# Kernel tuning notes

Hardware: AMD Instinct MI355X
Metric: run time of the kernel (lower is better)

The kernel has to match this reference:

```python
import jax, jax.numpy as jnp
import numpy as np

D_MODEL = 1024
N_HEADS = 16
HEAD_DIM = D_MODEL // N_HEADS
SCALE = HEAD_DIM ** -0.5
NEG = -9e15


def setup_inputs() -> dict:
    key = jax.random.key(0)
    k1, k2, k3 = jax.random.split(key, 3)
    B, S = 4, 2048
    x = jax.random.normal(k1, (B, S, D_MODEL), dtype=jnp.float32)
    W_qkv = jax.random.normal(k2, (D_MODEL, 3 * D_MODEL), dtype=jnp.float32) * (D_MODEL ** -0.5)
    b_qkv = jnp.zeros((3 * D_MODEL,), dtype=jnp.float32)
    W_out = jax.random.normal(k3, (D_MODEL, D_MODEL), dtype=jnp.float32) * (D_MODEL ** -0.5)
    b_out = jnp.zeros((D_MODEL,), dtype=jnp.float32)
    return {"x": x, "W_qkv": W_qkv, "b_qkv": b_qkv, "W_out": W_out, "b_out": b_out}


def reference(x, W_qkv, b_qkv, W_out, b_out):
    B, S, _ = x.shape
    qkv = x @ W_qkv + b_qkv                      # [B,S,3D]
    q, k, v = jnp.split(qkv, 3, axis=-1)
    def heads(t):
        return t.reshape(B, S, N_HEADS, HEAD_DIM).transpose(0, 2, 1, 3)  # [B,H,S,d]
    q, k, v = heads(q), heads(k), heads(v)
    logits = jnp.einsum('bhqd,bhkd->bhqk', q, k) * SCALE
    causal = jnp.tril(jnp.ones((S, S), dtype=bool))
    logits = jnp.where(causal[None, None], logits, jnp.float32(NEG))
    attn = jax.nn.softmax(logits, axis=-1)       # dropout p=0 -> identity
    vals = jnp.einsum('bhqk,bhkd->bhqd', attn, v)
    vals = vals.transpose(0, 2, 1, 3).reshape(B, S, D_MODEL)
    return vals @ W_out + b_out
```

## Files before the change

### kernel.cpp

```cpp
#include <hip/hip_runtime.h>

typedef unsigned short u16;
typedef unsigned int u32;
typedef __attribute__((ext_vector_type(8))) short bf16x8;
typedef __attribute__((ext_vector_type(4))) float f32x4;

#define MFMA16(a, b, c) __builtin_amdgcn_mfma_f32_16x16x32_bf16((a), (b), (c), 0, 0, 0)

constexpr int D = 1024;
constexpr int NH = 16;
constexpr int HD = 64;
constexpr int BB = 4;
constexpr int SS = 2048;
constexpr int BH = BB * NH;
constexpr int MTOK = BB * SS;
constexpr float SCALE_LOG2E = 0.125f * 1.44269504088896340736f;

__device__ __forceinline__ u16 f32_bf16(float f) {
  union { float f; u32 u; } v; v.f = f;
  u32 u = v.u;
  u += 0x7FFFu + ((u >> 16) & 1u);
  return (u16)(u >> 16);
}

__device__ __forceinline__ float exp2_fast(float x) {
  float r; asm("v_exp_f32 %0, %1" : "=v"(r) : "v"(x)); return r;
}
__device__ __forceinline__ u16 cvt_bf16_1(float f) {
  u32 r; asm("v_cvt_pk_bf16_f32 %0, %1, %1" : "=v"(r) : "v"(f)); return (u16)r;
}
__device__ __forceinline__ u32 cvt_pk2(float lo, float hi) {
  u32 r; asm("v_cvt_pk_bf16_f32 %0, %1, %2" : "=v"(r) : "v"(lo), "v"(hi)); return r;
}

__device__ __forceinline__ void gload_lds16(const void* g, u16* l) {
  __builtin_amdgcn_global_load_lds(
      (const __attribute__((address_space(1))) u32*)g,
      (__attribute__((address_space(3))) u32*)l, 16, 0, 0);
}

__global__ __launch_bounds__(256)
void cvt_bf16(const float* __restrict__ in, u16* __restrict__ out, int n4) {
  int i = blockIdx.x * 256 + threadIdx.x;
  const int stride = gridDim.x * 256;
  for (; i < n4; i += stride) {
    float4 v = reinterpret_cast<const float4*>(in)[i];
    u32 lo = (u32)f32_bf16(v.x) | ((u32)f32_bf16(v.y) << 16);
    u32 hi = (u32)f32_bf16(v.z) | ((u32)f32_bf16(v.w) << 16);
    reinterpret_cast<uint2*>(out)[i] = make_uint2(lo, hi);
  }
}

__global__ __launch_bounds__(256)
void transpose_bf16(const float* __restrict__ in, u16* __restrict__ out, int R, int C) {
  __shared__ float tile[32][33];
  const int c0 = blockIdx.x * 32, r0 = blockIdx.y * 32;
  const int tx = threadIdx.x, ty = threadIdx.y;
#pragma unroll
  for (int i = 0; i < 4; i++)
    tile[ty + 8 * i][tx] = in[(size_t)(r0 + ty + 8 * i) * C + c0 + tx];
  __syncthreads();
#pragma unroll
  for (int i = 0; i < 4; i++)
    out[(size_t)(c0 + ty + 8 * i) * R + r0 + tx] = f32_bf16(tile[tx][ty + 8 * i]);
}

template <int MODE>
__global__ __launch_bounds__(256)
void gemm_bf16(const u16* __restrict__ A, const u16* __restrict__ Bt,
               const float* __restrict__ bias,
               u16* __restrict__ q_out, u16* __restrict__ k_out,
               u16* __restrict__ vt_out, float* __restrict__ f_out,
               int M, int N, int K) {
  constexpr int BK = 32;
  __shared__ u16 lds_a[3][128 * BK];
  __shared__ u16 lds_b[3][128 * BK];
  const int m0 = blockIdx.x * 128;
  const int n0 = blockIdx.y * 128;
  const int t = threadIdx.x;
  const int lane = t & 63;
  const int w = t >> 6;
  const int wr = w >> 1, wc = w & 1;
  const int fr = lane & 15, fq = lane >> 4;

  const int srow = t >> 2;
  const int schunk = (t & 3) ^ ((srow >> 1) & 3);
  const u16* ga0 = A + (size_t)(m0 + srow) * K + schunk * 8;
  const u16* ga1 = ga0 + (size_t)64 * K;
  const u16* gb0 = Bt + (size_t)(n0 + srow) * K + schunk * 8;
  const u16* gb1 = gb0 + (size_t)64 * K;

  const int swz = ((fr >> 1) & 3) << 4;

#define GSTAGE(bufi, koff)                                                    \
  {                                                                           \
    gload_lds16(ga0 + (koff), lds_a[bufi] + t * 8);                           \
    gload_lds16(ga1 + (koff), lds_a[bufi] + (t + 256) * 8);                   \
    gload_lds16(gb0 + (koff), lds_b[bufi] + t * 8);                           \
    gload_lds16(gb1 + (koff), lds_b[bufi] + (t + 256) * 8);                   \
  }

  f32x4 acc[4][4] = {};
  const int nt = K / BK;

  GSTAGE(0, 0);
  GSTAGE(1, BK);

  int cur = 0;
  for (int kt = 0; kt < nt; ++kt) {
    if (kt + 1 < nt)
      asm volatile("s_waitcnt vmcnt(4)" ::: "memory");
    else
      asm volatile("s_waitcnt vmcnt(0)" ::: "memory");
    __builtin_amdgcn_s_barrier();
    __builtin_amdgcn_sched_barrier(0);

    const char* ca = (const char*)lds_a[cur];
    const char* cb = (const char*)lds_b[cur];
    bf16x8 af[4], bfr[4];
#pragma unroll
    for (int i = 0; i < 4; i++)
      af[i] = *reinterpret_cast<const bf16x8*>(
          ca + (wr * 64 + i * 16 + fr) * 64 + ((fq * 16) ^ swz));
#pragma unroll
    for (int i = 0; i < 4; i++)
      bfr[i] = *reinterpret_cast<const bf16x8*>(
          cb + (wc * 64 + i * 16 + fr) * 64 + ((fq * 16) ^ swz));
    __builtin_amdgcn_s_setprio(1);
#pragma unroll
    for (int i = 0; i < 4; i++)
#pragma unroll
      for (int j = 0; j < 4; j++)
        acc[i][j] = MFMA16(af[i], bfr[j], acc[i][j]);
    __builtin_amdgcn_s_setprio(0);

    if (kt + 2 < nt) {
      const int bufn = cur >= 1 ? cur - 1 : 2;
      GSTAGE(bufn, (kt + 2) * BK);
    }
    cur = cur == 2 ? 0 : cur + 1;
  }
#undef GSTAGE

#pragma unroll
  for (int i = 0; i < 4; i++) {
#pragma unroll
    for (int j = 0; j < 4; j++) {
      const int ncol = n0 + wc * 64 + j * 16 + fr;
      const float bs = bias[ncol];
#pragma unroll
      for (int r = 0; r < 4; r++) {
        const int mrow = m0 + wr * 64 + i * 16 + fq * 4 + r;
        const float vv = acc[i][j][r] + bs;
        if (MODE == 0) {
          const int which = ncol >> 10;
          const int rem = ncol & 1023;
          const int hh = rem >> 6, dd = rem & 63;
          const int bb = mrow >> 11, ss = mrow & 2047;
          const int bh = bb * 16 + hh;
          if (which == 0)
            q_out[((size_t)bh * SS + ss) * HD + dd] = f32_bf16(vv * SCALE_LOG2E);
          else if (which == 1)
            k_out[((size_t)bh * SS + ss) * HD + dd] = f32_bf16(vv);
          else
            vt_out[((size_t)bh * HD + dd) * SS + ss] = f32_bf16(vv);
        } else {
          f_out[(size_t)mrow * N + ncol] = vv;
        }
      }
    }
  }
}

__global__ __launch_bounds__(512)
void attn_fwd(const u16* __restrict__ Qb, const u16* __restrict__ Kb,
              const u16* __restrict__ Vt, u16* __restrict__ vals) {
  const int bid = blockIdx.x;
  const int wk = (bid & 7) * 64 + (bid >> 3);
  const int bh = wk >> 3;
  const int pA = wk & 7;
  const int qtA = pA, qtB = 15 - pA;
  const int nA = 2 * qtA + 2;
  const int nTot = 34;
  const u16* Qp = Qb + (size_t)bh * SS * HD;
  const char* Kp = (const char*)(Kb + (size_t)bh * SS * HD);
  const char* Vp = (const char*)(Vt + (size_t)bh * HD * SS);
  const int t = threadIdx.x, lane = t & 63, w = t >> 6;
  const int fr = lane & 15, fq = lane >> 4;
  const int swz = (fr & 7) << 4;

  __shared__ u16 kbuf[3][4096];
  __shared__ u16 vbuf[3][4096];
  __shared__ u16 plds[8][16][72];
  u16* myp = &plds[w][0][0];

  const int lin = t * 16;

  int offKV[8];
#pragma unroll
  for (int kf = 0; kf < 4; kf++)
#pragma unroll
    for (int kk = 0; kk < 2; kk++)
      offKV[kf * 2 + kk] = (kf * 16 + fr) * 128 + ((kk * 64 + fq * 16) ^ swz);

  bf16x8 aq[2];
  {
    const int qbase = qtA * 128 + w * 16;
#pragma unroll
    for (int kk = 0; kk < 2; kk++)
      aq[kk] = *reinterpret_cast<const bf16x8*>(Qp + (size_t)(qbase + fr) * HD + kk * 32 + fq * 8);
  }

  f32x4 o[4] = {};
  float mrun = -3e38f, lpart = 0.f;

#define STAGE(bufi, kvt_)                                                     \
  {                                                                           \
    const int row = lin >> 7, colb = lin & 127;                               \
    const int scol = colb ^ ((row & 7) << 4);                                 \
    gload_lds16(Kp + (size_t)((kvt_) * 64 + row) * 128 + scol,                \
                &kbuf[bufi][lin >> 1]);                                       \
    gload_lds16(Vp + (size_t)row * 4096 + (kvt_) * 128 + scol,                \
                &vbuf[bufi][lin >> 1]);                                       \
  }
#define KVIDX(ti_) ((ti_) >= nA ? (ti_) - nA : (ti_))

  auto write_out = [&](int qt) {
    const int b_ = bh >> 4, h_ = bh & 15;
    const int qb = qt * 128 + w * 16;
    float rs = lpart;
    rs += __shfl_xor(rs, 16, 64);
    rs += __shfl_xor(rs, 32, 64);
    const float linv = 1.f / rs;
    float lj[4];
#pragma unroll
    for (int j = 0; j < 4; j++)
      lj[j] = __shfl(linv, (lane & 48) + fq * 4 + j, 64);
#pragma unroll
    for (int df = 0; df < 4; df++)
#pragma unroll
      for (int j = 0; j < 4; j++) {
        const float vv = o[df][j] * lj[j];
        const int qg = qb + fq * 4 + j;
        vals[((size_t)(b_ * SS + qg)) * D + h_ * HD + df * 16 + fr] = cvt_bf16_1(vv);
      }
  };

  int cur = 0;
  STAGE(0, 0);
  STAGE(1, 1);

  for (int ti = 0; ti < nTot; ++ti) {
    const bool segB = ti >= nA;
    const int kvt = segB ? ti - nA : ti;
    const int qt = segB ? qtB : qtA;

    if (ti + 1 < nTot)
      asm volatile("s_waitcnt vmcnt(2)" ::: "memory");
    else
      asm volatile("s_waitcnt vmcnt(0)" ::: "memory");
    __builtin_amdgcn_s_barrier();
    __builtin_amdgcn_sched_barrier(0);

    if (ti == nA) {
      write_out(qtA);
      const int qbase = qtB * 128 + w * 16;
#pragma unroll
      for (int kk = 0; kk < 2; kk++)
        aq[kk] = *reinterpret_cast<const bf16x8*>(Qp + (size_t)(qbase + fr) * HD + kk * 32 + fq * 8);
      mrun = -3e38f; lpart = 0.f;
#pragma unroll
      for (int df = 0; df < 4; df++) o[df] = f32x4{0.f, 0.f, 0.f, 0.f};
    }

    const char* kb = (const char*)kbuf[cur];
    const char* vb = (const char*)vbuf[cur];

    f32x4 sc[4] = {};
    __builtin_amdgcn_s_setprio(1);
#pragma unroll
    for (int kf = 0; kf < 4; kf++) {
#pragma unroll
      for (int kk = 0; kk < 2; kk++) {
        bf16x8 bk = *reinterpret_cast<const bf16x8*>(kb + offKV[kf * 2 + kk]);
        sc[kf] = MFMA16(bk, aq[kk], sc[kf]);
      }
    }
    __builtin_amdgcn_s_setprio(0);
    if ((kvt >> 1) == qt) {
      const int qg = qt * 128 + w * 16 + fr;
      const int kg0 = kvt * 64 + fq * 4;
#pragma unroll
      for (int kf = 0; kf < 4; kf++)
#pragma unroll
        for (int j = 0; j < 4; j++)
          if (kg0 + kf * 16 + j > qg) sc[kf][j] = -3e38f;
    }
    float m = fmaxf(fmaxf(sc[0][0], sc[0][1]), fmaxf(sc[0][2], sc[0][3]));
#pragma unroll
    for (int kf = 1; kf < 4; kf++)
      m = fmaxf(m, fmaxf(fmaxf(sc[kf][0], sc[kf][1]), fmaxf(sc[kf][2], sc[kf][3])));
    m = fmaxf(m, __shfl_xor(m, 16, 64));
    m = fmaxf(m, __shfl_xor(m, 32, 64));
    if (__any((int)(m > mrun + 8.f))) {
      const float mnew = fmaxf(mrun, m);
      const float alpha = exp2_fast(mrun - mnew);
      mrun = mnew;
      lpart *= alpha;
      float aj[4];
#pragma unroll
      for (int j = 0; j < 4; j++)
        aj[j] = __shfl(alpha, (lane & 48) + fq * 4 + j, 64);
#pragma unroll
      for (int df = 0; df < 4; df++)
#pragma unroll
        for (int j = 0; j < 4; j++) o[df][j] *= aj[j];
    }
#pragma unroll
    for (int kf = 0; kf < 4; kf++)
#pragma unroll
      for (int j = 0; j < 4; j++) {
        const float p = exp2_fast(sc[kf][j] - mrun);
        sc[kf][j] = p;
        lpart += p;
      }
    {
      u16* mypr = myp + fr * 72;
#pragma unroll
      for (int kf = 0; kf < 4; kf++) {
        const u32 p01 = cvt_pk2(sc[kf][0], sc[kf][1]);
        const u32 p23 = cvt_pk2(sc[kf][2], sc[kf][3]);
        *reinterpret_cast<u32*>(mypr + kf * 16 + fq * 4) = p01;
        *reinterpret_cast<u32*>(mypr + kf * 16 + fq * 4 + 2) = p23;
      }
    }
    bf16x8 pa[2];
#pragma unroll
    for (int kk = 0; kk < 2; kk++)
      pa[kk] = *reinterpret_cast<const bf16x8*>(myp + fr * 72 + kk * 32 + fq * 8);
    __builtin_amdgcn_s_setprio(1);
#pragma unroll
    for (int df = 0; df < 4; df++) {
#pragma unroll
      for (int kk = 0; kk < 2; kk++) {
        bf16x8 bv = *reinterpret_cast<const bf16x8*>(vb + offKV[df * 2 + kk]);
        o[df] = MFMA16(pa[kk], bv, o[df]);
      }
    }
    __builtin_amdgcn_s_setprio(0);

    const int nxt = ti + 2;
    if (nxt < nTot) {
      const int bufn = cur >= 1 ? cur - 1 : 2;
      STAGE(bufn, KVIDX(nxt));
    }
    cur = cur == 2 ? 0 : cur + 1;
  }
  write_out(qtB);
#undef STAGE
#undef KVIDX
}

extern "C" void kernel_launch(void* const* d_in, const int* in_sizes, int n_in,
                              void* d_out, int out_size, void* d_ws, size_t ws_size,
                              hipStream_t stream) {
  const float* x = (const float*)d_in[0];
  const float* Wqkv = (const float*)d_in[1];
  const float* bqkv = (const float*)d_in[2];
  const float* Wout = (const float*)d_in[3];
  const float* bout = (const float*)d_in[4];
  float* out = (float*)d_out;

  char* p = (char*)d_ws;
  u16* xb = (u16*)p;    p += (size_t)MTOK * D * 2;
  u16* wqkvT = (u16*)p; p += (size_t)3 * D * D * 2;
  u16* woutT = (u16*)p; p += (size_t)D * D * 2;
  u16* Qb = (u16*)p;    p += (size_t)BH * SS * HD * 2;
  u16* Kb = (u16*)p;    p += (size_t)BH * SS * HD * 2;
  u16* Vt = (u16*)p;    p += (size_t)BH * SS * HD * 2;
  u16* vals = (u16*)p;  p += (size_t)MTOK * D * 2;

  cvt_bf16<<<2048, 256, 0, stream>>>(x, xb, MTOK * D / 4);
  transpose_bf16<<<dim3(3 * D / 32, D / 32), dim3(32, 8), 0, stream>>>(Wqkv, wqkvT, D, 3 * D);
  transpose_bf16<<<dim3(D / 32, D / 32), dim3(32, 8), 0, stream>>>(Wout, woutT, D, D);
  gemm_bf16<0><<<dim3(MTOK / 128, 3 * D / 128), 256, 0, stream>>>(
      xb, wqkvT, bqkv, Qb, Kb, Vt, nullptr, MTOK, 3 * D, D);
  attn_fwd<<<dim3(512), 512, 0, stream>>>(Qb, Kb, Vt, vals);
  gemm_bf16<1><<<dim3(MTOK / 128, D / 128), 256, 0, stream>>>(
      vals, woutT, bout, nullptr, nullptr, nullptr, out, MTOK, D, D);
}
```

Before: 171.8 us.

## Load GEMM B operand directly from global into registers, bypassing LDS

Stops staging the B (weight) tile in shared memory: each wave now loads its B fragments straight from global memory into registers, one k-step ahead, using double-buffered register sets. The A tile keeps its triple-buffered LDS pipeline, and the loop is unrolled by two to alternate the register buffers. This removes the B-side LDS traffic and halves the GEMM's shared-memory footprint, which could allow higher occupancy. In exchange, waves that share a column block load the same B data redundantly, the global access pattern is less coalesced (64-byte row segments), and register pressure rises.

```diff
diff --git a/kernel.cpp b/kernel.cpp
--- a/kernel.cpp
+++ b/kernel.cpp
@@ -74,7 +74,6 @@
                int M, int N, int K) {
   constexpr int BK = 32;
   __shared__ u16 lds_a[3][128 * BK];
-  __shared__ u16 lds_b[3][128 * BK];
   const int m0 = blockIdx.x * 128;
   const int n0 = blockIdx.y * 128;
   const int t = threadIdx.x;
@@ -87,60 +86,70 @@
   const int schunk = (t & 3) ^ ((srow >> 1) & 3);
   const u16* ga0 = A + (size_t)(m0 + srow) * K + schunk * 8;
   const u16* ga1 = ga0 + (size_t)64 * K;
-  const u16* gb0 = Bt + (size_t)(n0 + srow) * K + schunk * 8;
-  const u16* gb1 = gb0 + (size_t)64 * K;
+
+  const u16* gb[4];
+#pragma unroll
+  for (int j = 0; j < 4; j++)
+    gb[j] = Bt + (size_t)(n0 + wc * 64 + j * 16 + fr) * K + fq * 8;
 
   const int swz = ((fr >> 1) & 3) << 4;
 
-#define GSTAGE(bufi, koff)                                                    \
+#define ASTAGE(bufi, koff)                                                    \
   {                                                                           \
     gload_lds16(ga0 + (koff), lds_a[bufi] + t * 8);                           \
     gload_lds16(ga1 + (koff), lds_a[bufi] + (t + 256) * 8);                   \
-    gload_lds16(gb0 + (koff), lds_b[bufi] + t * 8);                           \
-    gload_lds16(gb1 + (koff), lds_b[bufi] + (t + 256) * 8);                   \
   }
 
   f32x4 acc[4][4] = {};
   const int nt = K / BK;
 
-  GSTAGE(0, 0);
-  GSTAGE(1, BK);
+  bf16x8 b0[4], b1[4];
+#pragma unroll
+  for (int j = 0; j < 4; j++)
+    b0[j] = *reinterpret_cast<const bf16x8*>(gb[j]);
+  ASTAGE(0, 0);
+  ASTAGE(1, BK);
 
   int cur = 0;
-  for (int kt = 0; kt < nt; ++kt) {
-    if (kt + 1 < nt)
-      asm volatile("s_waitcnt vmcnt(4)" ::: "memory");
-    else
-      asm volatile("s_waitcnt vmcnt(0)" ::: "memory");
-    __builtin_amdgcn_s_barrier();
-    __builtin_amdgcn_sched_barrier(0);
-
-    const char* ca = (const char*)lds_a[cur];
-    const char* cb = (const char*)lds_b[cur];
-    bf16x8 af[4], bfr[4];
-#pragma unroll
-    for (int i = 0; i < 4; i++)
-      af[i] = *reinterpret_cast<const bf16x8*>(
-          ca + (wr * 64 + i * 16 + fr) * 64 + ((fq * 16) ^ swz));
-#pragma unroll
-    for (int i = 0; i < 4; i++)
-      bfr[i] = *reinterpret_cast<const bf16x8*>(
-          cb + (wc * 64 + i * 16 + fr) * 64 + ((fq * 16) ^ swz));
-    __builtin_amdgcn_s_setprio(1);
-#pragma unroll
-    for (int i = 0; i < 4; i++)
-#pragma unroll
-      for (int j = 0; j < 4; j++)
-        acc[i][j] = MFMA16(af[i], bfr[j], acc[i][j]);
-    __builtin_amdgcn_s_setprio(0);
-
-    if (kt + 2 < nt) {
-      const int bufn = cur >= 1 ? cur - 1 : 2;
-      GSTAGE(bufn, (kt + 2) * BK);
-    }
-    cur = cur == 2 ? 0 : cur + 1;
-  }
-#undef GSTAGE
+#define GSTEP(kt, BUSE, BNEXT)                                                \
+  {                                                                           \
+    if ((kt) + 1 < nt)                                                        \
+      asm volatile("s_waitcnt vmcnt(6)" ::: "memory");                        \
+    else                                                                      \
+      asm volatile("s_waitcnt vmcnt(4)" ::: "memory");                        \
+    __builtin_amdgcn_s_barrier();                                             \
+    __builtin_amdgcn_sched_barrier(0);                                        \
+    if ((kt) + 1 < nt) {                                                      \
+      _Pragma("unroll")                                                       \
+      for (int j = 0; j < 4; j++)                                             \
+        BNEXT[j] = *reinterpret_cast<const bf16x8*>(gb[j] + ((kt) + 1) * BK); \
+    }                                                                         \
+    if ((kt) + 2 < nt) {                                                      \
+      const int bufn = cur >= 1 ? cur - 1 : 2;                 \
+      ASTAGE(bufn, ((kt) + 2) * BK);                                          \
+    }                                                                         \
+    const char* ca = (const char*)lds_a[cur];                                 \
+    bf16x8 af[4];                                                             \
+    _Pragma("unroll")                                                         \
+    for (int i = 0; i < 4; i++)                                               \
+      af[i] = *reinterpret_cast<const bf16x8*>(                               \
+          ca + (wr * 64 + i * 16 + fr) * 64 + ((fq * 16) ^ swz));             \
+    __builtin_amdgcn_s_setprio(1);                                            \
+    _Pragma("unroll")                                                         \
+    for (int i = 0; i < 4; i++)                                               \
+      _Pragma("unroll")                                                       \
+      for (int j = 0; j < 4; j++)                                             \
+        acc[i][j] = MFMA16(af[i], BUSE[j], acc[i][j]);                        \
+    __builtin_amdgcn_s_setprio(0);                                            \
+    cur = cur == 2 ? 0 : cur + 1;                                             \
+  }
+
+  for (int kt = 0; kt < nt; kt += 2) {
+    GSTEP(kt, b0, b1);
+    GSTEP(kt + 1, b1, b0);
+  }
+#undef GSTEP
+#undef ASTAGE
 
 #pragma unroll
   for (int i = 0; i < 4; i++) {
```

After: 231.8 us. +34.9%, slower.

## Enlarge GEMM tiles to 256x128 with BK=64 double buffering and vectorized V^T stores

Applied to the files above, without the earlier changes.

Moves the GEMM kernel from a 128x128 tile with 256 threads and a 3-stage BK=32 pipeline to a 256x128 tile with 512 threads and a 2-stage BK=64 pipeline. Each barrier now covers two k-substeps, and each B tile is reused across more rows of A. The QKV epilogue selects the output type once per block and packs the four V^T values into a single 8-byte store. The trade-offs are a shallower prefetch pipeline, more LDS per block (96KB), and half as many blocks, which may reduce occupancy.

```diff
diff --git a/kernel.cpp b/kernel.cpp
--- a/kernel.cpp
+++ b/kernel.cpp
@@ -66,16 +66,16 @@
 }
 
 template <int MODE>
-__global__ __launch_bounds__(256)
+__global__ __launch_bounds__(512)
 void gemm_bf16(const u16* __restrict__ A, const u16* __restrict__ Bt,
                const float* __restrict__ bias,
                u16* __restrict__ q_out, u16* __restrict__ k_out,
                u16* __restrict__ vt_out, float* __restrict__ f_out,
                int M, int N, int K) {
-  constexpr int BK = 32;
-  __shared__ u16 lds_a[3][128 * BK];
-  __shared__ u16 lds_b[3][128 * BK];
-  const int m0 = blockIdx.x * 128;
+  constexpr int BK = 64;
+  __shared__ u16 lds_a[2][16384];
+  __shared__ u16 lds_b[2][8192];
+  const int m0 = blockIdx.x * 256;
   const int n0 = blockIdx.y * 128;
   const int t = threadIdx.x;
   const int lane = t & 63;
@@ -84,32 +84,41 @@
   const int fr = lane & 15, fq = lane >> 4;
 
   const int srow = t >> 2;
-  const int schunk = (t & 3) ^ ((srow >> 1) & 3);
+  const int schunk = (t & 3) ^ ((t >> 3) & 3);
   const u16* ga0 = A + (size_t)(m0 + srow) * K + schunk * 8;
-  const u16* ga1 = ga0 + (size_t)64 * K;
+  const u16* ga1 = A + (size_t)(m0 + 128 + srow) * K + schunk * 8;
+  const u16* ga2 = ga0 + 32;
+  const u16* ga3 = ga1 + 32;
   const u16* gb0 = Bt + (size_t)(n0 + srow) * K + schunk * 8;
-  const u16* gb1 = gb0 + (size_t)64 * K;
-
-  const int swz = ((fr >> 1) & 3) << 4;
-
-#define GSTAGE(bufi, koff)                                                    \
+  const u16* gb1 = gb0 + 32;
+  const int t8 = t * 8;
+
+  const int rswz = ((fr >> 1) & 3) << 4;
+
+#define GSTAGE(bufi, kt)                                                      \
   {                                                                           \
-    gload_lds16(ga0 + (koff), lds_a[bufi] + t * 8);                           \
-    gload_lds16(ga1 + (koff), lds_a[bufi] + (t + 256) * 8);                   \
-    gload_lds16(gb0 + (koff), lds_b[bufi] + t * 8);                           \
-    gload_lds16(gb1 + (koff), lds_b[bufi] + (t + 256) * 8);                   \
+    const int ko = (kt)*BK;                                                   \
+    gload_lds16(ga0 + ko, lds_a[bufi] + t8);                                  \
+    gload_lds16(ga1 + ko, lds_a[bufi] + 4096 + t8);                           \
+    gload_lds16(ga2 + ko, lds_a[bufi] + 8192 + t8);                           \
+    gload_lds16(ga3 + ko, lds_a[bufi] + 12288 + t8);                          \
+    gload_lds16(gb0 + ko, lds_b[bufi] + t8);                                  \
+    gload_lds16(gb1 + ko, lds_b[bufi] + 4096 + t8);                           \
   }
 
   f32x4 acc[4][4] = {};
   const int nt = K / BK;
 
   GSTAGE(0, 0);
-  GSTAGE(1, BK);
-
   int cur = 0;
   for (int kt = 0; kt < nt; ++kt) {
+    if (kt) {
+      __builtin_amdgcn_s_barrier();
+      __builtin_amdgcn_sched_barrier(0);
+    }
+    if (kt + 1 < nt) GSTAGE(cur ^ 1, kt + 1);
     if (kt + 1 < nt)
-      asm volatile("s_waitcnt vmcnt(4)" ::: "memory");
+      asm volatile("s_waitcnt vmcnt(6)" ::: "memory");
     else
       asm volatile("s_waitcnt vmcnt(0)" ::: "memory");
     __builtin_amdgcn_s_barrier();
@@ -117,55 +126,70 @@
 
     const char* ca = (const char*)lds_a[cur];
     const char* cb = (const char*)lds_b[cur];
-    bf16x8 af[4], bfr[4];
-#pragma unroll
-    for (int i = 0; i < 4; i++)
-      af[i] = *reinterpret_cast<const bf16x8*>(
-          ca + (wr * 64 + i * 16 + fr) * 64 + ((fq * 16) ^ swz));
-#pragma unroll
-    for (int i = 0; i < 4; i++)
-      bfr[i] = *reinterpret_cast<const bf16x8*>(
-          cb + (wc * 64 + i * 16 + fr) * 64 + ((fq * 16) ^ swz));
-    __builtin_amdgcn_s_setprio(1);
-#pragma unroll
-    for (int i = 0; i < 4; i++)
+#pragma unroll
+    for (int ks = 0; ks < 2; ks++) {
+      bf16x8 af[4], bf[4];
+#pragma unroll
+      for (int i = 0; i < 4; i++)
+        af[i] = *reinterpret_cast<const bf16x8*>(
+            ca + ks * 16384 + (wr * 64 + i * 16 + fr) * 64 + ((fq * 16) ^ rswz));
 #pragma unroll
       for (int j = 0; j < 4; j++)
-        acc[i][j] = MFMA16(af[i], bfr[j], acc[i][j]);
-    __builtin_amdgcn_s_setprio(0);
-
-    if (kt + 2 < nt) {
-      const int bufn = cur >= 1 ? cur - 1 : 2;
-      GSTAGE(bufn, (kt + 2) * BK);
-    }
-    cur = cur == 2 ? 0 : cur + 1;
+        bf[j] = *reinterpret_cast<const bf16x8*>(
+            cb + ks * 8192 + (wc * 64 + j * 16 + fr) * 64 + ((fq * 16) ^ rswz));
+      __builtin_amdgcn_s_setprio(1);
+#pragma unroll
+      for (int i = 0; i < 4; i++)
+#pragma unroll
+        for (int j = 0; j < 4; j++)
+          acc[i][j] = MFMA16(af[i], bf[j], acc[i][j]);
+      __builtin_amdgcn_s_setprio(0);
+    }
+    cur ^= 1;
   }
 #undef GSTAGE
 
-#pragma unroll
-  for (int i = 0; i < 4; i++) {
-#pragma unroll
-    for (int j = 0; j < 4; j++) {
-      const int ncol = n0 + wc * 64 + j * 16 + fr;
-      const float bs = bias[ncol];
-#pragma unroll
-      for (int r = 0; r < 4; r++) {
-        const int mrow = m0 + wr * 64 + i * 16 + fq * 4 + r;
-        const float vv = acc[i][j][r] + bs;
-        if (MODE == 0) {
-          const int which = ncol >> 10;
-          const int rem = ncol & 1023;
-          const int hh = rem >> 6, dd = rem & 63;
-          const int bb = mrow >> 11, ss = mrow & 2047;
-          const int bh = bb * 16 + hh;
-          if (which == 0)
-            q_out[((size_t)bh * SS + ss) * HD + dd] = f32_bf16(vv * SCALE_LOG2E);
-          else if (which == 1)
-            k_out[((size_t)bh * SS + ss) * HD + dd] = f32_bf16(vv);
-          else
-            vt_out[((size_t)bh * HD + dd) * SS + ss] = f32_bf16(vv);
+  if (MODE == 0) {
+    const int swhich = n0 >> 10;
+#pragma unroll
+    for (int i = 0; i < 4; i++) {
+#pragma unroll
+      for (int j = 0; j < 4; j++) {
+        const int ncol = n0 + wc * 64 + j * 16 + fr;
+        const float bs = bias[ncol];
+        const int rem = ncol & 1023;
+        const int hh = rem >> 6, dd = rem & 63;
+        const int mbase = m0 + wr * 64 + i * 16 + fq * 4;
+        const int bb = mbase >> 11, ss = mbase & 2047;
+        const int bh = bb * 16 + hh;
+        if (swhich == 0) {
+#pragma unroll
+          for (int r = 0; r < 4; r++)
+            q_out[((size_t)bh * SS + ss + r) * HD + dd] =
+                f32_bf16((acc[i][j][r] + bs) * SCALE_LOG2E);
+        } else if (swhich == 1) {
+#pragma unroll
+          for (int r = 0; r < 4; r++)
+            k_out[((size_t)bh * SS + ss + r) * HD + dd] = f32_bf16(acc[i][j][r] + bs);
         } else {
-          f_out[(size_t)mrow * N + ncol] = vv;
+          const u32 p01 = cvt_pk2(acc[i][j][0] + bs, acc[i][j][1] + bs);
+          const u32 p23 = cvt_pk2(acc[i][j][2] + bs, acc[i][j][3] + bs);
+          *reinterpret_cast<uint2*>(&vt_out[((size_t)bh * HD + dd) * SS + ss]) =
+              make_uint2(p01, p23);
+        }
+      }
+    }
+  } else {
+#pragma unroll
+    for (int i = 0; i < 4; i++) {
+#pragma unroll
+      for (int j = 0; j < 4; j++) {
+        const int ncol = n0 + wc * 64 + j * 16 + fr;
+        const float bs = bias[ncol];
+#pragma unroll
+        for (int r = 0; r < 4; r++) {
+          const int mrow = m0 + wr * 64 + i * 16 + fq * 4 + r;
+          f_out[(size_t)mrow * N + ncol] = acc[i][j][r] + bs;
         }
       }
     }
@@ -383,9 +407,9 @@
   cvt_bf16<<<2048, 256, 0, stream>>>(x, xb, MTOK * D / 4);
   transpose_bf16<<<dim3(3 * D / 32, D / 32), dim3(32, 8), 0, stream>>>(Wqkv, wqkvT, D, 3 * D);
   transpose_bf16<<<dim3(D / 32, D / 32), dim3(32, 8), 0, stream>>>(Wout, woutT, D, D);
-  gemm_bf16<0><<<dim3(MTOK / 128, 3 * D / 128), 256, 0, stream>>>(
+  gemm_bf16<0><<<dim3(MTOK / 256, 3 * D / 128), 512, 0, stream>>>(
       xb, wqkvT, bqkv, Qb, Kb, Vt, nullptr, MTOK, 3 * D, D);
   attn_fwd<<<dim3(512), 512, 0, stream>>>(Qb, Kb, Vt, vals);
-  gemm_bf16<1><<<dim3(MTOK / 128, D / 128), 256, 0, stream>>>(
+  gemm_bf16<1><<<dim3(MTOK / 256, D / 128), 512, 0, stream>>>(
       vals, woutT, bout, nullptr, nullptr, nullptr, out, MTOK, D, D);
 }
```

Result: slower. 179.0 us (+4.2%).

## Replace QKV GEMM with 256x256-tile 8-wave kernel using phased async LDS prefetch

Applied to the files above, without the earlier changes.

Adds a dedicated QKV projection kernel that uses 256x256 output tiles, 512 threads and BK=64, with an XOR-swizzled LDS layout. Each k-step is split into four quarter-phases, and each phase issues the next staging load directly from global memory to LDS, so loads overlap with MFMA work across double buffers. The intent is more data reuse per block and better latency hiding than the 128x128 generic GEMM. In exchange the kernel carries 128 accumulators per thread, which raises register pressure and lowers occupancy, and the grid is only 32x12 blocks.

```diff
diff --git a/kernel.cpp b/kernel.cpp
--- a/kernel.cpp
+++ b/kernel.cpp
@@ -63,6 +63,125 @@
 #pragma unroll
   for (int i = 0; i < 4; i++)
     out[(size_t)(c0 + ty + 8 * i) * R + r0 + tx] = f32_bf16(tile[tx][ty + 8 * i]);
+}
+
+__global__ __launch_bounds__(512)
+void gemm_qkv_8ph(const u16* __restrict__ A, const u16* __restrict__ Bt,
+                  const float* __restrict__ bias,
+                  u16* __restrict__ q_out, u16* __restrict__ k_out,
+                  u16* __restrict__ vt_out) {
+  constexpr int K = 1024, BK = 64, NT = K / BK;
+  __shared__ u16 ldsA[2][2][128 * 64];
+  __shared__ u16 ldsB[2][2][128 * 64];
+  const int m0 = blockIdx.x * 256;
+  const int n0 = blockIdx.y * 256;
+  const int t = threadIdx.x, lane = t & 63, w = t >> 6;
+  const int wr = w >> 2, wc = w & 3;
+  const int fr = lane & 15, fq = lane >> 4;
+  const int rsw = fr & 7;
+
+  const int srow = t >> 3;
+  const int sch = (t & 7) ^ (srow & 7);
+  const u16* gA0 = A + (size_t)(m0 + srow) * K + sch * 8;
+  const u16* gA1 = A + (size_t)(m0 + 128 + srow) * K + sch * 8;
+  const u16* gB0 = Bt + (size_t)(n0 + srow) * K + sch * 8;
+  const u16* gB1 = Bt + (size_t)(n0 + 128 + srow) * K + sch * 8;
+
+  auto stageH = [&](int H) {
+    const int kt = H >> 2, h = H & 3, par = kt & 1, ko = kt * BK;
+    u16* base; const u16* src;
+    if (h == 0)      { base = &ldsA[par][0][0]; src = gA0; }
+    else if (h == 1) { base = &ldsA[par][1][0]; src = gA1; }
+    else if (h == 2) { base = &ldsB[par][0][0]; src = gB0; }
+    else             { base = &ldsB[par][1][0]; src = gB1; }
+    gload_lds16(src + ko, base + t * 8);
+    gload_lds16(src + (size_t)64 * K + ko, base + (t + 512) * 8);
+  };
+
+  f32x4 acc[8][4] = {};
+
+  for (int H = 0; H < 5; ++H) stageH(H);
+  asm volatile("s_waitcnt vmcnt(2)" ::: "memory");
+  __builtin_amdgcn_s_barrier();
+  __builtin_amdgcn_sched_barrier(0);
+
+  bf16x8 af[4][2], bf[2][2];
+  for (int kt = 0; kt < NT; ++kt) {
+    const int par = kt & 1;
+    const char* cA = (const char*)&ldsA[par][wr][0];
+    const char* cB = (const char*)&ldsB[par][wc >> 1][0];
+    const int brow = (wc & 1) * 64;
+#pragma unroll
+    for (int q = 0; q < 4; ++q) {
+      const int mi = q >> 1, nj = q & 1;
+      if (nj == 0) {
+#pragma unroll
+        for (int i = 0; i < 4; i++)
+#pragma unroll
+          for (int ks = 0; ks < 2; ks++)
+            af[i][ks] = *reinterpret_cast<const bf16x8*>(
+                cA + ((mi * 4 + i) * 16 + fr) * 128 + (((ks * 4 + fq) ^ rsw) << 4));
+      }
+#pragma unroll
+      for (int j = 0; j < 2; j++)
+#pragma unroll
+        for (int ks = 0; ks < 2; ks++)
+          bf[j][ks] = *reinterpret_cast<const bf16x8*>(
+              cB + (brow + (nj * 2 + j) * 16 + fr) * 128 + (((ks * 4 + fq) ^ rsw) << 4));
+      const int H = kt * 4 + q + 5;
+      if (H < NT * 4) stageH(H);
+      __builtin_amdgcn_s_barrier();
+      __builtin_amdgcn_sched_barrier(0);
+      __builtin_amdgcn_s_setprio(1);
+#pragma unroll
+      for (int i = 0; i < 4; i++)
+#pragma unroll
+        for (int j = 0; j < 2; j++)
+#pragma unroll
+          for (int ks = 0; ks < 2; ks++)
+            acc[mi * 4 + i][nj * 2 + j] =
+                MFMA16(af[i][ks], bf[j][ks], acc[mi * 4 + i][nj * 2 + j]);
+      __builtin_amdgcn_s_setprio(0);
+      if (q == 3) {
+        if (kt + 2 < NT)
+          asm volatile("s_waitcnt vmcnt(2)" ::: "memory");
+        else if (kt + 1 < NT)
+          asm volatile("s_waitcnt vmcnt(0)" ::: "memory");
+      }
+      __builtin_amdgcn_s_barrier();
+      __builtin_amdgcn_sched_barrier(0);
+    }
+  }
+
+  const int swhich = n0 >> 10;
+#pragma unroll
+  for (int i = 0; i < 8; i++) {
+#pragma unroll
+    for (int j = 0; j < 4; j++) {
+      const int ncol = n0 + wc * 64 + j * 16 + fr;
+      const float bs = bias[ncol];
+      const int rem = ncol & 1023;
+      const int hh = rem >> 6, dd = rem & 63;
+      const int mbase = m0 + wr * 128 + i * 16 + fq * 4;
+      const int bb = mbase >> 11, ss = mbase & 2047;
+      const int bh = bb * 16 + hh;
+      if (swhich == 0) {
+#pragma unroll
+        for (int r = 0; r < 4; r++)
+          q_out[((size_t)bh * SS + ss + r) * HD + dd] =
+              f32_bf16((acc[i][j][r] + bs) * SCALE_LOG2E);
+      } else if (swhich == 1) {
+#pragma unroll
+        for (int r = 0; r < 4; r++)
+          k_out[((size_t)bh * SS + ss + r) * HD + dd] = f32_bf16(acc[i][j][r] + bs);
+      } else {
+        const u32 p01 = cvt_pk2(acc[i][j][0] + bs, acc[i][j][1] + bs);
+        const u32 p23 = cvt_pk2(acc[i][j][2] + bs, acc[i][j][3] + bs);
+        *reinterpret_cast<uint2*>(&vt_out[((size_t)bh * HD + dd) * SS + ss]) =
+            make_uint2(p01, p23);
+      }
+    }
+  }
 }
 
 template <int MODE>
@@ -383,8 +502,8 @@
   cvt_bf16<<<2048, 256, 0, stream>>>(x, xb, MTOK * D / 4);
   transpose_bf16<<<dim3(3 * D / 32, D / 32), dim3(32, 8), 0, stream>>>(Wqkv, wqkvT, D, 3 * D);
   transpose_bf16<<<dim3(D / 32, D / 32), dim3(32, 8), 0, stream>>>(Wout, woutT, D, D);
-  gemm_bf16<0><<<dim3(MTOK / 128, 3 * D / 128), 256, 0, stream>>>(
-      xb, wqkvT, bqkv, Qb, Kb, Vt, nullptr, MTOK, 3 * D, D);
+  gemm_qkv_8ph<<<dim3(MTOK / 256, 3 * D / 256), 512, 0, stream>>>(
+      xb, wqkvT, bqkv, Qb, Kb, Vt);
   attn_fwd<<<dim3(512), 512, 0, stream>>>(Qb, Kb, Vt, vals);
   gemm_bf16<1><<<dim3(MTOK / 128, D / 128), 256, 0, stream>>>(
       vals, woutT, bout, nullptr, nullptr, nullptr, out, MTOK, D, D);
```

Result: slower. 176.5 us (+2.7%).
